# Optimization experiments

Measured on AMD Instinct MI355X. Metric: run time of the kernel, lower is better.

Reference implementation:

```python
import jax, jax.numpy as jnp
import numpy as np

N_NODES = 20000
N_EDGES = 240000
NUM_SPECIES = 4
NUM_BASIS = 16
MAX_RADIUS = 3.15
SQRT_NN = float(np.sqrt(12.0))  # num_neighbors normalization


def _cg121():
    # Clebsch-Gordan for 1e x 2e -> 1e in the real l=2 basis used below:
    # [xy, yz, (3z^2-1), zx, x^2-y^2] (component-normalized). Built from the
    # symmetric traceless matrix pairing M(a) @ v, normalized to unit Frobenius norm.
    s5, s15 = np.sqrt(5.0), np.sqrt(15.0)
    C = np.zeros((3, 5, 3))
    for A in range(5):
        a = np.zeros(5); a[A] = 1.0
        M = np.zeros((3, 3))
        M[0, 1] = M[1, 0] = a[0] * s15 / 2
        M[1, 2] = M[2, 1] = a[1] * s15 / 2
        M[0, 2] = M[2, 0] = a[3] * s15 / 2
        M[0, 0] = -a[2] * s5 / 2 + a[4] * s15 / 2
        M[1, 1] = -a[2] * s5 / 2 - a[4] * s15 / 2
        M[2, 2] = a[2] * s5
        C[:, A, :] = M
    C /= np.linalg.norm(C)
    return jnp.asarray(C, dtype=jnp.float32)

CG121 = _cg121()


def silu(v):
    return v * jax.nn.sigmoid(v)


def lin0(h, W):  # equivariant linear on scalars: [N,u] x [u,v]
    return h @ W / np.sqrt(W.shape[0])


def lin1(h, W):  # equivariant linear on vectors: [N,u,3] x [u,v]
    return jnp.einsum('nuk,uv->nvk', h, W) / np.sqrt(W.shape[0])


def radial_mlp(hb, W1, W2):  # FullyConnectedNet([16,64,nw], silu), normalized weights
    h = silu(hb @ W1 / np.sqrt(W1.shape[0]))
    return h @ W2 / np.sqrt(W2.shape[0])


def radial_basis(r):
    # soft_one_hot_linspace(..., basis='smooth_finite', cutoff=True) * sqrt(NUM_BASIS)
    values = np.linspace(0.0, MAX_RADIUS, NUM_BASIS + 2, dtype=np.float32)[1:-1]
    step = float(values[1] - values[0])
    d = (r[:, None] - values) / step
    def sus(t):
        safe = jnp.where(t > 0, t, 1.0)
        return jnp.where(t > 0, jnp.exp(-1.0 / safe), 0.0)
    y = 1.14136 * float(np.exp(2.0)) * sus(1.0 + d) * sus(1.0 - d)
    return y * np.sqrt(float(NUM_BASIS))


def sph_harm(edge_vec):
    # normalize=True, normalization='component' real spherical harmonics, l=0,1,2
    r = jnp.linalg.norm(edge_vec, axis=1)
    u = edge_vec / r[:, None]
    ux, uy, uz = u[:, 0], u[:, 1], u[:, 2]
    sh1 = np.sqrt(3.0) * u
    sh2 = jnp.stack([np.sqrt(15.0) * ux * uy,
                     np.sqrt(15.0) * uy * uz,
                     np.sqrt(5.0) / 2 * (3 * uz * uz - 1.0),
                     np.sqrt(15.0) * uz * ux,
                     np.sqrt(15.0) / 2 * (ux * ux - uy * uy)], axis=1)
    return r, sh1, sh2


def _forward(x, edge_index, edge_vec, emb,
             L1_lin1_0, L1_W1, L1_W2, L1_lin2_0, L1_lin2_1, L1_sc_0,
             L2_lin1_0, L2_lin1_1, L2_W1, L2_W2, L2_lin2_0, L2_lin2_1, L2_sc_0, L2_sc_1,
             LO_lin1_0, LO_lin1_1, LO_W1, LO_W2, LO_lin2_0, LO_sc_0):
    src, dst = edge_index[0], edge_index[1]
    N = x.shape[0]
    h0 = emb[x]                                   # [N,64] node embedding
    r, sh1, sh2 = sph_harm(edge_vec)
    hb = radial_basis(r)                          # [E,16]

    # ---- interaction 1: 64x0e -> (144x0e + 16x1e) -> gate -> 128x0e + 16x1e
    sc0 = lin0(h0, L1_sc_0)                       # self-connection [N,144]
    x0 = lin0(h0, L1_lin1_0)[src]                 # [E,64]
    w = radial_mlp(hb, L1_W1, L1_W2)              # [E,128] TP weights (uvu)
    m0 = x0 * w[:, :64]                           # 0e x 0e -> 0e
    m1 = (x0 * w[:, 64:128])[:, :, None] * sh1[:, None, :]  # 0e x 1e -> 1e
    a0 = jax.ops.segment_sum(m0, dst, num_segments=N) / SQRT_NN
    a1 = jax.ops.segment_sum(m1, dst, num_segments=N) / SQRT_NN
    g0 = lin0(a0, L1_lin2_0) + sc0                # [N,144]
    g1 = lin1(a1, L1_lin2_1)                      # [N,16,3]
    h0 = silu(g0[:, :128])                        # gated scalars
    h1 = jax.nn.sigmoid(g0[:, 128:])[:, :, None] * g1  # gate 16x1e

    # ---- interaction 2: 128x0e+16x1e -> (144x0e + 176x1e mid) -> gate
    sc0 = lin0(h0, L2_sc_0)                       # [N,144]
    sc1 = lin1(h1, L2_sc_1)                       # [N,16,3]
    x0 = lin0(h0, L2_lin1_0)[src]                 # [E,128]
    x1 = lin1(h1, L2_lin1_1)[src]                 # [E,16,3]
    w = radial_mlp(hb, L2_W1, L2_W2)              # [E,320]
    m0a = x0 * w[:, :128]                                            # 0x0->0
    m0b = jnp.einsum('euk,ek->eu', x1, sh1) / np.sqrt(3.0) * w[:, 272:288]  # 1x1->0
    m1a = (x0 * w[:, 128:256])[:, :, None] * sh1[:, None, :]         # 0x1->1
    m1b = x1 * w[:, 256:272][:, :, None]                             # 1x0->1
    m1c = jnp.cross(x1, sh1[:, None, :]) / np.sqrt(6.0) * w[:, 288:304][:, :, None]  # 1x1->1
    m1d = jnp.einsum('eui,eA,iAk->euk', x1, sh2, CG121) * w[:, 304:320][:, :, None]  # 1x2->1
    mid0 = jnp.concatenate([m0a, m0b], axis=1)    # [E,144]
    mid1 = jnp.concatenate([m1a, m1b, m1c, m1d], axis=1)  # [E,176,3]
    a0 = jax.ops.segment_sum(mid0, dst, num_segments=N) / SQRT_NN
    a1 = jax.ops.segment_sum(mid1, dst, num_segments=N) / SQRT_NN
    g0 = lin0(a0, L2_lin2_0) + sc0
    g1 = lin1(a1, L2_lin2_1) + sc1
    h0 = silu(g0[:, :128])
    h1 = jax.nn.sigmoid(g0[:, 128:])[:, :, None] * g1

    # ---- output interaction: -> 4x0e
    sc0 = lin0(h0, LO_sc_0)                       # [N,4]
    x0 = lin0(h0, LO_lin1_0)[src]
    x1 = lin1(h1, LO_lin1_1)[src]
    w = radial_mlp(hb, LO_W1, LO_W2)              # [E,144]
    m0a = x0 * w[:, :128]
    m0b = jnp.einsum('euk,ek->eu', x1, sh1) / np.sqrt(3.0) * w[:, 128:144]
    a0 = jax.ops.segment_sum(jnp.concatenate([m0a, m0b], axis=1), dst, num_segments=N) / SQRT_NN
    return lin0(a0, LO_lin2_0) + sc0              # [N,4]


def setup_inputs() -> dict:
    key = jax.random.key(0)
    ks = jax.random.split(key, 32)
    f = lambda i, shape: jax.random.normal(ks[i], shape, dtype=jnp.float32)
    return {
        'x': jax.random.randint(ks[0], (N_NODES,), 0, NUM_SPECIES),
        'edge_index': jax.random.randint(ks[1], (2, N_EDGES), 0, N_NODES),
        'edge_vec': jax.random.normal(ks[2], (N_EDGES, 3), dtype=jnp.float32),
        'emb': f(3, (NUM_SPECIES, 64)),
        'L1_lin1_0': f(4, (64, 64)),
        'L1_W1': f(5, (16, 64)), 'L1_W2': f(6, (64, 128)),
        'L1_lin2_0': f(7, (64, 144)), 'L1_lin2_1': f(8, (64, 16)),
        'L1_sc_0': f(9, (64, 144)),
        'L2_lin1_0': f(10, (128, 128)), 'L2_lin1_1': f(11, (16, 16)),
        'L2_W1': f(12, (16, 64)), 'L2_W2': f(13, (64, 320)),
        'L2_lin2_0': f(14, (144, 144)), 'L2_lin2_1': f(15, (176, 16)),
        'L2_sc_0': f(16, (128, 144)), 'L2_sc_1': f(17, (16, 16)),
        'LO_lin1_0': f(18, (128, 128)), 'LO_lin1_1': f(19, (16, 16)),
        'LO_W1': f(20, (16, 64)), 'LO_W2': f(21, (64, 144)),
        'LO_lin2_0': f(22, (144, 4)), 'LO_sc_0': f(23, (128, 4)),
    }


def reference(x, edge_index, edge_vec, emb,
              L1_lin1_0, L1_W1, L1_W2, L1_lin2_0, L1_lin2_1, L1_sc_0,
              L2_lin1_0, L2_lin1_1, L2_W1, L2_W2, L2_lin2_0, L2_lin2_1, L2_sc_0, L2_sc_1,
              LO_lin1_0, LO_lin1_1, LO_W1, LO_W2, LO_lin2_0, LO_sc_0):
    return _forward(x, edge_index, edge_vec, emb,
                    L1_lin1_0, L1_W1, L1_W2, L1_lin2_0, L1_lin2_1, L1_sc_0,
                    L2_lin1_0, L2_lin1_1, L2_W1, L2_W2, L2_lin2_0, L2_lin2_1, L2_sc_0, L2_sc_1,
                    LO_lin1_0, LO_lin1_1, LO_W1, LO_W2, LO_lin2_0, LO_sc_0)
```

## Files before the change

kernel.cpp:

```cpp
#include <hip/hip_runtime.h>
#include <math.h>

#define N_NODES 20000
#define N_EDGES 240000

typedef _Float16 half2_t __attribute__((ext_vector_type(2)));
typedef _Float16 f16x8   __attribute__((ext_vector_type(8)));
typedef float    f32x4v  __attribute__((ext_vector_type(4)));
typedef unsigned uint4v  __attribute__((ext_vector_type(4)));

__device__ __forceinline__ float siluf(float v){ return v * (1.0f/(1.0f+__expf(-v))); }
__device__ __forceinline__ float sigmf(float v){ return 1.0f/(1.0f+__expf(-v)); }

__device__ __forceinline__ unsigned pack_h2(float a, float b){
  half2_t h; h.x = (_Float16)a; h.y = (_Float16)b;
  return __builtin_bit_cast(unsigned, h);
}
__device__ __forceinline__ float dot2f(unsigned w, unsigned h, float acc){
#if __has_builtin(__builtin_amdgcn_fdot2)
  return __builtin_amdgcn_fdot2(__builtin_bit_cast(half2_t,w),
                                __builtin_bit_cast(half2_t,h), acc, false);
#else
  half2_t a = __builtin_bit_cast(half2_t,w), b = __builtin_bit_cast(half2_t,h);
  return acc + (float)a.x*(float)b.x + (float)a.y*(float)b.y;
#endif
}
__device__ __forceinline__ float dot8q(uint4v w, uint4v h, float acc){
  acc = dot2f(w.x, h.x, acc);
  acc = dot2f(w.y, h.y, acc);
  acc = dot2f(w.z, h.z, acc);
  return dot2f(w.w, h.w, acc);
}

__global__ void k_count(const int* __restrict__ ei, int* __restrict__ cnt){
  int e = blockIdx.x*blockDim.x + threadIdx.x;
  if (e < N_EDGES) atomicAdd(&cnt[ei[N_EDGES + e]], 1);
}

__global__ void k_scan(const int* __restrict__ cnt, int* __restrict__ off, int* __restrict__ pos){
  __shared__ int part[1024];
  int t = threadIdx.x;
  int c[20]; int s = 0;
  #pragma unroll
  for (int j=0;j<20;j++){
    int idx = t*20 + j;
    int v = (idx < N_NODES) ? cnt[idx] : 0;
    c[j] = s; s += v;
  }
  part[t] = s;
  __syncthreads();
  for (int d=1; d<1024; d<<=1){
    int add = (t>=d) ? part[t-d] : 0;
    __syncthreads();
    part[t] += add;
    __syncthreads();
  }
  int excl = part[t] - s;
  #pragma unroll
  for (int j=0;j<20;j++){
    int idx = t*20 + j;
    if (idx < N_NODES){ off[idx] = excl + c[j]; pos[idx] = excl + c[j]; }
  }
  if (t == 1023) off[N_NODES] = part[1023];
}

__global__ void k_scatter(const int* __restrict__ ei, int* __restrict__ pos,
                          int* __restrict__ perm, int* __restrict__ srcs){
  int e = blockIdx.x*blockDim.x + threadIdx.x;
  if (e >= N_EDGES) return;
  int d = ei[N_EDGES + e];
  int p = atomicAdd(&pos[d], 1);
  perm[e] = p;
  srcs[p] = ei[e];
}

__global__ void k_geom(const float* __restrict__ ev, const int* __restrict__ perm,
                       float* __restrict__ eg){
  int e = blockIdx.x*blockDim.x + threadIdx.x;
  if (e >= N_EDGES) return;
  float x = ev[3*e+0], y = ev[3*e+1], z = ev[3*e+2];
  float r = sqrtf(x*x + y*y + z*z);
  float inv = 1.0f / fmaxf(r, 1e-12f);
  float ux = x*inv, uy = y*inv, uz = z*inv;
  float* o = eg + (size_t)perm[e]*24;
  o[0] = 1.7320508f*ux; o[1] = 1.7320508f*uy; o[2] = 1.7320508f*uz;
  o[3] = 3.8729833f*ux*uy;
  o[4] = 3.8729833f*uy*uz;
  o[5] = 1.1180340f*(3.0f*uz*uz - 1.0f);
  o[6] = 3.8729833f*uz*ux;
  o[7] = 1.9364917f*(ux*ux - uy*uy);
  const float invstep = 17.0f/3.15f;
  float t = r*invstep;
  #pragma unroll
  for (int i=0;i<16;i++){
    float d = t - (float)(i+1);
    float a = 1.0f + d, b = 1.0f - d;
    float v = 0.0f;
    if (a > 0.0f && b > 0.0f) v = 33.734292f*__expf(-1.0f/a - 1.0f/b);
    o[8+i] = v;
  }
}

__global__ void k_packw(const float* __restrict__ Wu,
                        const float* __restrict__ Ws,  const float* __restrict__ Wl,
                        const float* __restrict__ Wlo, const float* __restrict__ Wso,
                        unsigned* __restrict__ WPu,
                        unsigned* __restrict__ WPs,  unsigned* __restrict__ WPl,
                        unsigned* __restrict__ WPlo, unsigned* __restrict__ WPso){
  int i = blockIdx.x*blockDim.x + threadIdx.x;
  const float f12 = 1.0f/12.0f;
  const float is128 = 0.08838835f;
  if (i < 144*72){
    int t = i/72, k2 = i%72;
    WPu[i] = pack_h2(Wu[(2*k2)*144+t]*f12, Wu[(2*k2+1)*144+t]*f12);
  } else if (i < 144*72 + 144*64){
    int ii = i - 144*72; int t = ii/64, k2 = ii%64;
    WPs[ii] = pack_h2(Ws[(2*k2)*144+t]*is128, Ws[(2*k2+1)*144+t]*is128);
  } else if (i < 144*72 + 144*64 + 128*64){
    int ii = i - 144*72 - 144*64; int t = ii/64, k2 = ii%64;
    WPl[ii] = pack_h2(Wl[(2*k2)*128+t]*is128, Wl[(2*k2+1)*128+t]*is128);
  } else if (i < 144*72 + 144*64 + 128*64 + 128*64){
    int ii = i - 144*72 - 144*64 - 128*64; int t = ii/64, k2 = ii%64;
    WPlo[ii] = pack_h2(Wlo[(2*k2)*128+t]*is128, Wlo[(2*k2+1)*128+t]*is128);
  } else if (i < 144*72 + 144*64 + 128*64 + 128*64 + 4*64){
    int ii = i - 144*72 - 144*64 - 128*64 - 128*64; int t = ii/64, k2 = ii%64;
    WPso[ii] = pack_h2(Wso[(2*k2)*4+t]*is128, Wso[(2*k2+1)*4+t]*is128);
  }
}

__global__ void k_node_l1(const int* __restrict__ xs, const float* __restrict__ emb,
                          const float* __restrict__ Wlin, const float* __restrict__ Wsc,
                          _Float16* __restrict__ X0, float* __restrict__ SC0){
  __shared__ float hs[4][64];
  int n0 = blockIdx.x*4;
  int t  = threadIdx.x;
  {
    int j = t>>6, k = t&63;
    hs[j][k] = emb[xs[n0+j]*64 + k];
  }
  __syncthreads();
  if (t < 64){
    float acc[4] = {};
    for (int k=0;k<64;k++){
      float wv = Wlin[k*64 + t];
      #pragma unroll
      for (int j=0;j<4;j++) acc[j] += hs[j][k]*wv;
    }
    #pragma unroll
    for (int j=0;j<4;j++) X0[(size_t)(n0+j)*64 + t] = (_Float16)(acc[j]*0.125f);
  } else if (t < 208){
    int o = t - 64;
    float acc[4] = {};
    for (int k=0;k<64;k++){
      float wv = Wsc[k*144 + o];
      #pragma unroll
      for (int j=0;j<4;j++) acc[j] += hs[j][k]*wv;
    }
    #pragma unroll
    for (int j=0;j<4;j++) SC0[(size_t)(n0+j)*144 + o] = acc[j]*0.125f;
  }
}

__global__ __launch_bounds__(256) void k_hidden(
    const float* __restrict__ EG, const float* __restrict__ W1,
    _Float16* __restrict__ H){
  __shared__ float w1s[16*64];
  int tid = threadIdx.x;
  for (int i=tid;i<16*64;i+=256) w1s[i] = W1[i]*0.25f;
  __syncthreads();
  int lane = tid & 63, wib = tid >> 6;
  int gw = blockIdx.x*4 + wib, nw = gridDim.x*4;
  for (int e = gw; e < N_EDGES; e += nw){
    const float* g8 = EG + (size_t)e*24 + 8;
    float a0 = 0.0f, a1 = 0.0f;
    #pragma unroll
    for (int b=0;b<8;b++){
      a0 = fmaf(g8[b],   w1s[b*64 + lane],     a0);
      a1 = fmaf(g8[8+b], w1s[(8+b)*64 + lane], a1);
    }
    H[(size_t)e*64 + lane] = (_Float16)siluf(a0 + a1);
  }
}

template<int MODE>
__device__ __forceinline__ float colscale(int c){
  if constexpr (MODE == 1){
    if (c >= 272 && c < 288) return 0.57735027f;
    if (c >= 288 && c < 304) return 0.40824829f;
    return 1.0f;
  } else if constexpr (MODE == 2){
    return (c >= 128) ? 0.57735027f : 1.0f;
  }
  return 1.0f;
}

template<int NT, int MODE>
__global__ __launch_bounds__(256) void k_ww_mfma(
    int e0c, int e1c, const _Float16* __restrict__ H,
    const float* __restrict__ W2, _Float16* __restrict__ WW){
  constexpr int NCOL = NT*16;
  constexpr int NTW  = (NT + 3) / 4;
  int tid = threadIdx.x;
  int lane = tid & 63, wib = tid >> 6;
  int row = lane & 15, quad = lane >> 4;
  const float fold = 0.125f*0.28867513f;
  f16x8 B0[NTW], B1[NTW];
  #pragma unroll
  for (int t2=0; t2<NTW; t2++){
    int ct = wib*NTW + t2;
    int c  = ct*16 + row;
    bool valid = (ct < NT);
    float fs = valid ? fold*colscale<MODE>(c) : 0.0f;
    int ci = valid ? c : 0;
    #pragma unroll
    for (int j=0;j<8;j++){
      B0[t2][j] = (_Float16)(W2[(quad*8+j)*NCOL + ci]*fs);
      B1[t2][j] = (_Float16)(W2[(32+quad*8+j)*NCOL + ci]*fs);
    }
  }
  int ntiles = (e1c - e0c) >> 4;
  for (int t = blockIdx.x; t < ntiles; t += gridDim.x){
    int eb = e0c + t*16;
    const _Float16* hp = H + (size_t)(eb + row)*64 + quad*8;
    f16x8 A0 = *(const f16x8*)hp;
    f16x8 A1 = *(const f16x8*)(hp + 32);
    #pragma unroll
    for (int t2=0; t2<NTW; t2++){
      int ct = wib*NTW + t2;
      f32x4v d = __builtin_amdgcn_mfma_f32_16x16x32_f16(A0, B0[t2], (f32x4v){0.f,0.f,0.f,0.f}, 0,0,0);
      d = __builtin_amdgcn_mfma_f32_16x16x32_f16(A1, B1[t2], d, 0,0,0);
      if (ct < NT){
        int c0 = ct*16;
        #pragma unroll
        for (int j=0;j<4;j++){
          WW[(size_t)(eb - e0c + quad*4 + j)*NCOL + c0 + row] = (_Float16)d[j];
        }
      }
    }
  }
}

__global__ __launch_bounds__(256) void k_gather_l1(
    const int* __restrict__ off, const int* __restrict__ srcs, const float* __restrict__ eg,
    const _Float16* __restrict__ WW, const _Float16* __restrict__ X0,
    float* __restrict__ A0, float* __restrict__ A1, int e0, int e1, int first){
  int tid = threadIdx.x, lane = tid & 63;
  int gw = (blockIdx.x*256 + tid) >> 6;
  int nw = (gridDim.x*256) >> 6;
  for (int n = gw; n < N_NODES; n += nw){
    int ib = off[n], ie = off[n+1];
    if (ib < e0) ib = e0;
    if (ie > e1) ie = e1;
    if (!first && ib >= ie) continue;
    float a0a = 0.0f, a1a[3] = {0,0,0};
    if (ib < ie){
      int src = srcs[ib];
      for (int i = ib; i < ie; i++){
        float x0 = (float)X0[(size_t)src*64 + lane];
        if (i+1 < ie) src = srcs[i+1];
        const float* g = eg + (size_t)i*24;
        const _Float16* w = WW + (size_t)(i - e0)*128;
        float w0  = (float)w[lane];
        float w1v = (float)w[64 + lane];
        float m0 = x0*w0, m1 = x0*w1v;
        a0a += m0;
        a1a[0] += m1*g[0]; a1a[1] += m1*g[1]; a1a[2] += m1*g[2];
      }
    }
    float* p = A1 + (size_t)n*192 + lane*3;
    if (first){
      A0[(size_t)n*64 + lane] = a0a;
      p[0] = a1a[0]; p[1] = a1a[1]; p[2] = a1a[2];
    } else {
      A0[(size_t)n*64 + lane] += a0a;
      p[0] += a1a[0]; p[1] += a1a[1]; p[2] += a1a[2];
    }
  }
}

__global__ __launch_bounds__(256) void k_gather_l2(
    const int* __restrict__ off, const int* __restrict__ srcs, const float* __restrict__ eg,
    const _Float16* __restrict__ WW, const _Float16* __restrict__ X0, const _Float16* __restrict__ X1,
    float* __restrict__ A0, float* __restrict__ A1, int e0, int e1, int first){
  int tid = threadIdx.x, lane = tid & 63;
  int grp = lane >> 4, v = lane & 15;
  int gw = (blockIdx.x*256 + tid) >> 6;
  int nw = (gridDim.x*256) >> 6;
  for (int n = gw; n < N_NODES; n += nw){
    int ib = off[n], ie = off[n+1];
    if (ib < e0) ib = e0;
    if (ie > e1) ie = e1;
    if (!first && ib >= ie) continue;
    float a0a=0.f, a0b=0.f, a0c=0.f;
    float a1a[3]={0,0,0}, a1b[3]={0,0,0}, a1g[3]={0,0,0};
    if (ib < ie){
      int src = srcs[ib];
      for (int i = ib; i < ie; i++){
        const _Float16* x0p = X0 + (size_t)src*128;
        float x0a = (float)x0p[lane], x0b = (float)x0p[64 + lane];
        const _Float16* x1p = X1 + (size_t)src*48 + v*3;
        float xx = (float)x1p[0], xy = (float)x1p[1], xz = (float)x1p[2];
        if (i+1 < ie) src = srcs[i+1];
        const float* g = eg + (size_t)i*24;
        const _Float16* w = WW + (size_t)(i - e0)*320;
        float w0  = (float)w[lane];
        float w1v = (float)w[ 64 + lane];
        float w2v = (float)w[128 + lane];
        float w3v = (float)w[192 + lane];
        float w4  = (float)w[256 + lane];
        float sx = g[0], sy = g[1], sz = g[2];
        a0a += x0a*w0;
        a0b += x0b*w1v;
        float ma = x0a*w2v, mb = x0b*w3v;
        a1a[0] += ma*sx; a1a[1] += ma*sy; a1a[2] += ma*sz;
        a1b[0] += mb*sx; a1b[1] += mb*sy; a1b[2] += mb*sz;
        if (grp == 0){
          a1g[0] += w4*xx; a1g[1] += w4*xy; a1g[2] += w4*xz;
        } else if (grp == 1){
          a0c += w4*(xx*sx + xy*sy + xz*sz);
        } else if (grp == 2){
          a1g[0] += w4*(xy*sz - xz*sy);
          a1g[1] += w4*(xz*sx - xx*sz);
          a1g[2] += w4*(xx*sy - xy*sx);
        } else {
          float s20=g[3], s21=g[4], s22=g[5], s23=g[6], s24=g[7];
          const float c1c = 0.31622777f, c2c = 0.18257419f;
          a1g[0] += w4*(xx*(c1c*s24 - c2c*s22) + xy*(c1c*s20)            + xz*(c1c*s23));
          a1g[1] += w4*(xx*(c1c*s20)           + xy*(-c2c*s22 - c1c*s24) + xz*(c1c*s21));
          a1g[2] += w4*(xx*(c1c*s23)           + xy*(c1c*s21)            + xz*(2.0f*c2c*s22));
        }
      }
    }
    float* a0 = A0 + (size_t)n*144;
    float* a1 = A1 + (size_t)n*528;
    int gbase = (grp == 0) ? 128 : (grp == 2) ? 144 : (grp == 3) ? 160 : -1;
    if (first){
      a0[lane] = a0a;
      a0[64 + lane] = a0b;
      if (grp == 1) a0[128 + v] = a0c;
      float* p = a1 + lane*3;
      p[0] = a1a[0]; p[1] = a1a[1]; p[2] = a1a[2];
      p = a1 + (64 + lane)*3;
      p[0] = a1b[0]; p[1] = a1b[1]; p[2] = a1b[2];
      if (gbase >= 0){
        p = a1 + (gbase + v)*3;
        p[0] = a1g[0]; p[1] = a1g[1]; p[2] = a1g[2];
      }
    } else {
      a0[lane] += a0a;
      a0[64 + lane] += a0b;
      if (grp == 1) a0[128 + v] += a0c;
      float* p = a1 + lane*3;
      p[0] += a1a[0]; p[1] += a1a[1]; p[2] += a1a[2];
      p = a1 + (64 + lane)*3;
      p[0] += a1b[0]; p[1] += a1b[1]; p[2] += a1b[2];
      if (gbase >= 0){
        p = a1 + (gbase + v)*3;
        p[0] += a1g[0]; p[1] += a1g[1]; p[2] += a1g[2];
      }
    }
  }
}

__global__ __launch_bounds__(256) void k_gather_lo(
    const int* __restrict__ off, const int* __restrict__ srcs, const float* __restrict__ eg,
    const _Float16* __restrict__ WW, const _Float16* __restrict__ X0, const _Float16* __restrict__ X1,
    float* __restrict__ A0, int e0, int e1, int first){
  int tid = threadIdx.x, lane = tid & 63, v = lane & 15;
  int gw = (blockIdx.x*256 + tid) >> 6;
  int nw = (gridDim.x*256) >> 6;
  for (int n = gw; n < N_NODES; n += nw){
    int ib = off[n], ie = off[n+1];
    if (ib < e0) ib = e0;
    if (ie > e1) ie = e1;
    if (!first && ib >= ie) continue;
    float a0a = 0.f, a0b = 0.f, a0c = 0.f;
    if (ib < ie){
      int src = srcs[ib];
      for (int i = ib; i < ie; i++){
        const _Float16* x0p = X0 + (size_t)src*128;
        float x0a = (float)x0p[lane], x0b = (float)x0p[64 + lane];
        const _Float16* x1p = X1 + (size_t)src*48 + v*3;
        float xx = (float)x1p[0], xy = (float)x1p[1], xz = (float)x1p[2];
        if (i+1 < ie) src = srcs[i+1];
        const float* g = eg + (size_t)i*24;
        const _Float16* w = WW + (size_t)(i - e0)*144;
        float w0  = (float)w[lane];
        float w1v = (float)w[64 + lane];
        float w2v = (float)w[128 + v];
        a0a += x0a*w0;
        a0b += x0b*w1v;
        float dot = xx*g[0] + xy*g[1] + xz*g[2];
        a0c += w2v*dot;
      }
    }
    float* a0 = A0 + (size_t)n*144;
    if (first){
      a0[lane] = a0a;
      a0[64 + lane] = a0b;
      if (lane < 16) a0[128 + lane] = a0c;
    } else {
      a0[lane] += a0a;
      a0[64 + lane] += a0b;
      if (lane < 16) a0[128 + lane] += a0c;
    }
  }
}

__global__ __launch_bounds__(256) void k_upd_l1(
    const float* __restrict__ A0, const float* __restrict__ A1,
    const float* __restrict__ SC0,
    const float* __restrict__ W20, const float* __restrict__ W21,
    float* __restrict__ H0, float* __restrict__ H1){
  __shared__ float a0s[8*64];
  __shared__ float a1s[8*192];
  __shared__ float w21s[64*16];
  __shared__ float sig[8][16];
  __shared__ float g1s[8][48];
  int n0 = blockIdx.x*8, t = threadIdx.x;
  {
    const float4* s0 = (const float4*)(A0 + (size_t)n0*64);
    float4* d0 = (float4*)a0s;
    for (int i=t;i<8*64/4;i+=256) d0[i] = s0[i];
    const float4* s1 = (const float4*)(A1 + (size_t)n0*192);
    float4* d1 = (float4*)a1s;
    for (int i=t;i<8*192/4;i+=256) d1[i] = s1[i];
    const float4* sw = (const float4*)W21;
    float4* dw = (float4*)w21s;
    for (int i=t;i<64*16/4;i+=256) dw[i] = sw[i];
  }
  __syncthreads();
  if (t < 144){
    float acc[8] = {};
    for (int k=0;k<64;k++){
      float wv = W20[k*144 + t];
      #pragma unroll
      for (int j=0;j<8;j++) acc[j] += a0s[j*64 + k]*wv;
    }
    #pragma unroll
    for (int j=0;j<8;j++){
      float gg = acc[j]*0.125f + SC0[(size_t)(n0+j)*144 + t];
      if (t < 128) H0[(size_t)(n0+j)*128 + t] = siluf(gg);
      else         sig[j][t-128] = sigmf(gg);
    }
  } else if (t < 192){
    int idx = t-144, v = idx/3, k = idx%3;
    float acc[8] = {};
    for (int u=0;u<64;u++){
      float wv = w21s[u*16 + v];
      #pragma unroll
      for (int j=0;j<8;j++) acc[j] += a1s[j*192 + u*3 + k]*wv;
    }
    #pragma unroll
    for (int j=0;j<8;j++) g1s[j][idx] = acc[j]*0.125f;
  }
  __syncthreads();
  if (t >= 144 && t < 192){
    int idx = t-144, v = idx/3;
    #pragma unroll
    for (int j=0;j<8;j++) H1[(size_t)(n0+j)*48 + idx] = sig[j][v]*g1s[j][idx];
  }
}

__global__ __launch_bounds__(384) void k_lin_l2(
    const float* __restrict__ H0, const float* __restrict__ H1,
    const unsigned* __restrict__ WPs, const float* __restrict__ Wsc1,
    const unsigned* __restrict__ WPl, const float* __restrict__ Wl1,
    float* __restrict__ SC0, float* __restrict__ SC1,
    _Float16* __restrict__ X0,  _Float16* __restrict__ X1){
  __shared__ uint4v h0h8[128];
  __shared__ float h1s[8*48];
  int n0 = blockIdx.x*8, t = threadIdx.x;
  if (t < 128){
    const float4* s0 = (const float4*)(H0 + (size_t)n0*128);
    float4 f0 = s0[t*2], f1 = s0[t*2+1];
    uint4v u;
    u.x = pack_h2(f0.x, f0.y); u.y = pack_h2(f0.z, f0.w);
    u.z = pack_h2(f1.x, f1.y); u.w = pack_h2(f1.z, f1.w);
    h0h8[t] = u;
  } else if (t < 224){
    int i = t - 128;
    const float4* s1 = (const float4*)(H1 + (size_t)n0*48);
    if (i < 96) ((float4*)h1s)[i] = s1[i];
  }
  __syncthreads();
  const uint4v* wps4 = (const uint4v*)WPs;
  const uint4v* wpl4 = (const uint4v*)WPl;
  if (t < 144){
    float acc[8] = {};
    for (int kq=0;kq<16;kq++){
      uint4v wq = wps4[t*16 + kq];
      #pragma unroll
      for (int j=0;j<8;j++){
        uint4v av = h0h8[j*16 + kq];
        acc[j] = dot8q(wq, av, acc[j]);
      }
    }
    #pragma unroll
    for (int j=0;j<8;j++) SC0[(size_t)(n0+j)*144 + t] = acc[j];
  } else if (t < 192){
    int idx = t-144, v = idx/3, k = idx%3;
    float acc[8] = {};
    for (int u=0;u<16;u++){
      float wv = Wsc1[u*16 + v];
      #pragma unroll
      for (int j=0;j<8;j++) acc[j] += h1s[j*48 + u*3 + k]*wv;
    }
    #pragma unroll
    for (int j=0;j<8;j++) SC1[(size_t)(n0+j)*48 + idx] = acc[j]*0.25f;
  } else if (t < 320){
    int o = t-192;
    float acc[8] = {};
    for (int kq=0;kq<16;kq++){
      uint4v wq = wpl4[o*16 + kq];
      #pragma unroll
      for (int j=0;j<8;j++){
        uint4v av = h0h8[j*16 + kq];
        acc[j] = dot8q(wq, av, acc[j]);
      }
    }
    #pragma unroll
    for (int j=0;j<8;j++) X0[(size_t)(n0+j)*128 + o] = (_Float16)acc[j];
  } else if (t < 368){
    int idx = t-320, v = idx/3, k = idx%3;
    float acc[8] = {};
    for (int u=0;u<16;u++){
      float wv = Wl1[u*16 + v];
      #pragma unroll
      for (int j=0;j<8;j++) acc[j] += h1s[j*48 + u*3 + k]*wv;
    }
    #pragma unroll
    for (int j=0;j<8;j++) X1[(size_t)(n0+j)*48 + idx] = (_Float16)(acc[j]*0.25f);
  }
}

__global__ __launch_bounds__(256) void k_upd_l2(
    const float* __restrict__ A0, const float* __restrict__ A1,
    const float* __restrict__ SC0, const float* __restrict__ SC1,
    const unsigned* __restrict__ WPu, const float* __restrict__ W21,
    float* __restrict__ H0, float* __restrict__ H1){
  __shared__ uint4v a0h8[144];
  __shared__ float a1s[8*528];
  __shared__ float sig[8][16];
  __shared__ float g1s[8][48];
  int n0 = blockIdx.x*8, t = threadIdx.x;
  if (t < 144){
    const float4* s0 = (const float4*)(A0 + (size_t)n0*144);
    float4 f0 = s0[t*2], f1 = s0[t*2+1];
    uint4v u;
    u.x = pack_h2(f0.x, f0.y); u.y = pack_h2(f0.z, f0.w);
    u.z = pack_h2(f1.x, f1.y); u.w = pack_h2(f1.z, f1.w);
    a0h8[t] = u;
  }
  {
    const float4* s1 = (const float4*)(A1 + (size_t)n0*528);
    float4* d1 = (float4*)a1s;
    for (int i=t;i<8*528/4;i+=256) d1[i] = s1[i];
  }
  __syncthreads();
  const uint4v* wpu4 = (const uint4v*)WPu;
  if (t < 144){
    float acc[8] = {};
    for (int kq=0;kq<18;kq++){
      uint4v wq = wpu4[t*18 + kq];
      #pragma unroll
      for (int j=0;j<8;j++){
        uint4v av = a0h8[j*18 + kq];
        acc[j] = dot8q(wq, av, acc[j]);
      }
    }
    #pragma unroll
    for (int j=0;j<8;j++){
      float gg = acc[j] + SC0[(size_t)(n0+j)*144 + t];
      if (t < 128) H0[(size_t)(n0+j)*128 + t] = siluf(gg);
      else         sig[j][t-128] = sigmf(gg);
    }
  } else if (t < 192){
    int idx = t-144, v = idx/3, k = idx%3;
    float acc[8] = {};
    for (int u=0;u<176;u++){
      float wv = W21[u*16 + v];
      #pragma unroll
      for (int j=0;j<8;j++) acc[j] += a1s[j*528 + u*3 + k]*wv;
    }
    #pragma unroll
    for (int j=0;j<8;j++) g1s[j][idx] = acc[j]*0.075377836f + SC1[(size_t)(n0+j)*48 + idx];
  }
  __syncthreads();
  if (t >= 144 && t < 192){
    int idx = t-144, v = idx/3;
    #pragma unroll
    for (int j=0;j<8;j++) H1[(size_t)(n0+j)*48 + idx] = sig[j][v]*g1s[j][idx];
  }
}

__global__ __launch_bounds__(256) void k_lin_lo(
    const float* __restrict__ H0, const float* __restrict__ H1,
    const unsigned* __restrict__ WPso,
    const unsigned* __restrict__ WPlo, const float* __restrict__ Wl1,
    float* __restrict__ SCO, _Float16* __restrict__ X0, _Float16* __restrict__ X1){
  __shared__ uint4v h0h8[128];
  __shared__ float h1s[8*48];
  int n0 = blockIdx.x*8, t = threadIdx.x;
  if (t < 128){
    const float4* s0 = (const float4*)(H0 + (size_t)n0*128);
    float4 f0 = s0[t*2], f1 = s0[t*2+1];
    uint4v u;
    u.x = pack_h2(f0.x, f0.y); u.y = pack_h2(f0.z, f0.w);
    u.z = pack_h2(f1.x, f1.y); u.w = pack_h2(f1.z, f1.w);
    h0h8[t] = u;
  } else if (t < 224){
    int i = t - 128;
    const float4* s1 = (const float4*)(H1 + (size_t)n0*48);
    if (i < 96) ((float4*)h1s)[i] = s1[i];
  }
  __syncthreads();
  const uint4v* wso4 = (const uint4v*)WPso;
  const uint4v* wlo4 = (const uint4v*)WPlo;
  if (t < 4){
    float acc[8] = {};
    for (int kq=0;kq<16;kq++){
      uint4v wq = wso4[t*16 + kq];
      #pragma unroll
      for (int j=0;j<8;j++){
        uint4v av = h0h8[j*16 + kq];
        acc[j] = dot8q(wq, av, acc[j]);
      }
    }
    #pragma unroll
    for (int j=0;j<8;j++) SCO[(size_t)(n0+j)*4 + t] = acc[j];
  } else if (t < 132){
    int o = t-4;
    float acc[8] = {};
    for (int kq=0;kq<16;kq++){
      uint4v wq = wlo4[o*16 + kq];
      #pragma unroll
      for (int j=0;j<8;j++){
        uint4v av = h0h8[j*16 + kq];
        acc[j] = dot8q(wq, av, acc[j]);
      }
    }
    #pragma unroll
    for (int j=0;j<8;j++) X0[(size_t)(n0+j)*128 + o] = (_Float16)acc[j];
  } else if (t < 180){
    int idx = t-132, v = idx/3, k = idx%3;
    float acc[8] = {};
    for (int u=0;u<16;u++){
      float wv = Wl1[u*16 + v];
      #pragma unroll
      for (int j=0;j<8;j++) acc[j] += h1s[j*48 + u*3 + k]*wv;
    }
    #pragma unroll
    for (int j=0;j<8;j++) X1[(size_t)(n0+j)*48 + idx] = (_Float16)(acc[j]*0.25f);
  }
}

__global__ __launch_bounds__(256) void k_final(
    const float* __restrict__ A0, const float* __restrict__ SCO,
    const float* __restrict__ W, float* __restrict__ out){
  __shared__ float a0s[32*144];
  int n0 = blockIdx.x*32, t = threadIdx.x;
  {
    const float4* s0 = (const float4*)(A0 + (size_t)n0*144);
    float4* d0 = (float4*)a0s;
    for (int i=t;i<32*144/4;i+=256) d0[i] = s0[i];
  }
  __syncthreads();
  if (t < 128){
    int j = t >> 2, c = t & 3;
    float acc = 0.0f;
    for (int k=0;k<144;k++) acc += a0s[j*144 + k]*W[k*4 + c];
    int i = (n0 + j)*4 + c;
    out[i] = acc*(1.0f/12.0f) + SCO[i];
  }
}

extern "C" void kernel_launch(void* const* d_in, const int* in_sizes, int n_in,
                              void* d_out, int out_size, void* d_ws, size_t ws_size,
                              hipStream_t stream) {
  const int*   x   = (const int*)  d_in[0];
  const int*   ei  = (const int*)  d_in[1];
  const float* ev  = (const float*)d_in[2];
  const float* emb = (const float*)d_in[3];
  const float* L1_lin1_0 = (const float*)d_in[4];
  const float* L1_W1     = (const float*)d_in[5];
  const float* L1_W2     = (const float*)d_in[6];
  const float* L1_lin2_0 = (const float*)d_in[7];
  const float* L1_lin2_1 = (const float*)d_in[8];
  const float* L1_sc_0   = (const float*)d_in[9];
  const float* L2_lin1_0 = (const float*)d_in[10];
  const float* L2_lin1_1 = (const float*)d_in[11];
  const float* L2_W1     = (const float*)d_in[12];
  const float* L2_W2     = (const float*)d_in[13];
  const float* L2_lin2_0 = (const float*)d_in[14];
  const float* L2_lin2_1 = (const float*)d_in[15];
  const float* L2_sc_0   = (const float*)d_in[16];
  const float* L2_sc_1   = (const float*)d_in[17];
  const float* LO_lin1_0 = (const float*)d_in[18];
  const float* LO_lin1_1 = (const float*)d_in[19];
  const float* LO_W1     = (const float*)d_in[20];
  const float* LO_W2     = (const float*)d_in[21];
  const float* LO_lin2_0 = (const float*)d_in[22];
  const float* LO_sc_0   = (const float*)d_in[23];
  float* out = (float*)d_out;

  int* cnt  = (int*)d_ws;
  int* off  = cnt  + N_NODES;
  int* pos  = off  + N_NODES + 1;
  int* perm = pos  + N_NODES;
  int* srcs = perm + N_EDGES;
  float* EG  = (float*)(((char*)d_ws) + ((size_t)540004 * 4));
  _Float16* X0 = (_Float16*)(EG + (size_t)N_EDGES*24);
  _Float16* X1 = (_Float16*)(X0 + (size_t)N_NODES*128);
  float* SC0 = (float*)(((char*)(X1 + (size_t)N_NODES*48)) + 0);
  float* SC1 = SC0 + (size_t)N_NODES*144;
  float* A0  = SC1 + (size_t)N_NODES*48;
  float* A1  = A0  + (size_t)N_NODES*144;
  float* H0  = A1  + (size_t)N_NODES*528;
  float* H1  = H0  + (size_t)N_NODES*128;
  _Float16* HH = (_Float16*)(H1 + (size_t)N_NODES*48);
  unsigned* WPu  = (unsigned*)(HH + (size_t)N_EDGES*64);
  unsigned* WPs  = WPu  + 144*72;
  unsigned* WPl  = WPs  + 144*64;
  unsigned* WPlo = WPl  + 128*64;
  unsigned* WPso = WPlo + 128*64;
  _Float16* WW = (_Float16*)(WPso + 4*64);

  size_t used = (size_t)((char*)WW - (char*)d_ws);
  size_t avail = (ws_size > used) ? (ws_size - used) : 0;
  auto chunk_for = [&](int ncol)->int{
    size_t ce = avail / ((size_t)ncol * sizeof(_Float16));
    if (ce >= (size_t)N_EDGES) return N_EDGES;
    int c = (int)ce & ~15;
    return c < 4096 ? 4096 : c;
  };

  hipMemsetAsync(cnt, 0, N_NODES*sizeof(int), stream);
  k_count  <<<(N_EDGES+255)/256, 256, 0, stream>>>(ei, cnt);
  k_scan   <<<1, 1024, 0, stream>>>(cnt, off, pos);
  k_scatter<<<(N_EDGES+255)/256, 256, 0, stream>>>(ei, pos, perm, srcs);
  k_geom   <<<(N_EDGES+255)/256, 256, 0, stream>>>(ev, perm, EG);
  k_packw  <<<142, 256, 0, stream>>>(L2_lin2_0, L2_sc_0, L2_lin1_0,
                                     LO_lin1_0, LO_sc_0,
                                     WPu, WPs, WPl, WPlo, WPso);

  k_node_l1<<<N_NODES/4, 256, 0, stream>>>(x, emb, L1_lin1_0, L1_sc_0, X0, SC0);
  k_hidden<<<2048, 256, 0, stream>>>(EG, L1_W1, HH);
  {
    int chunk = chunk_for(128);
    for (int e0 = 0; e0 < N_EDGES; e0 += chunk){
      int e1 = (e0 + chunk < N_EDGES) ? e0 + chunk : N_EDGES;
      k_ww_mfma<8,0><<<2048, 256, 0, stream>>>(e0, e1, HH, L1_W2, WW);
      k_gather_l1<<<5000, 256, 0, stream>>>(off, srcs, EG, WW, X0, A0, A1, e0, e1, e0==0);
    }
  }
  k_upd_l1<<<N_NODES/8, 256, 0, stream>>>(A0, A1, SC0, L1_lin2_0, L1_lin2_1, H0, H1);

  k_lin_l2<<<N_NODES/8, 384, 0, stream>>>(H0, H1, WPs, L2_sc_1, WPl, L2_lin1_1,
                                          SC0, SC1, X0, X1);
  k_hidden<<<2048, 256, 0, stream>>>(EG, L2_W1, HH);
  {
    int chunk = chunk_for(320);
    for (int e0 = 0; e0 < N_EDGES; e0 += chunk){
      int e1 = (e0 + chunk < N_EDGES) ? e0 + chunk : N_EDGES;
      k_ww_mfma<20,1><<<2048, 256, 0, stream>>>(e0, e1, HH, L2_W2, WW);
      k_gather_l2<<<5000, 256, 0, stream>>>(off, srcs, EG, WW, X0, X1, A0, A1, e0, e1, e0==0);
    }
  }
  k_upd_l2<<<N_NODES/8, 256, 0, stream>>>(A0, A1, SC0, SC1, WPu, L2_lin2_1, H0, H1);

  k_lin_lo<<<N_NODES/8, 256, 0, stream>>>(H0, H1, WPso, WPlo, LO_lin1_1, SC1, X0, X1);
  k_hidden<<<2048, 256, 0, stream>>>(EG, LO_W1, HH);
  {
    int chunk = chunk_for(144);
    for (int e0 = 0; e0 < N_EDGES; e0 += chunk){
      int e1 = (e0 + chunk < N_EDGES) ? e0 + chunk : N_EDGES;
      k_ww_mfma<9,2><<<2048, 256, 0, stream>>>(e0, e1, HH, LO_W2, WW);
      k_gather_lo<<<5000, 256, 0, stream>>>(off, srcs, EG, WW, X0, X1, A0, e0, e1, e0==0);
    }
  }
  k_final<<<N_NODES/32, 256, 0, stream>>>(A0, SC1, LO_lin2_0, out);
}
```

Baseline: 623.6 us.

## Interleave fp16 node and edge-weight layouts for paired loads in gathers

Node features X0 are stored with the two 64-channel halves interleaved, X1 vectors are padded to 4 halves, and the MFMA edge-weight writer interleaves column blocks in pairs. This lets the gather kernels fetch two fp16 values with one 32-bit load (or 64-bit for X1) instead of separate scalar half loads. The l=2 spherical harmonics are also precomputed in k_geom as the symmetric CG matrix entries, which removes per-lane arithmetic in the gather. The cost is a larger X1 buffer and scattered 16-bit stores in the MFMA and node kernels.

```diff
diff --git a/kernel.cpp b/kernel.cpp
--- a/kernel.cpp
+++ b/kernel.cpp
@@ -15,6 +15,10 @@
 __device__ __forceinline__ unsigned pack_h2(float a, float b){
   half2_t h; h.x = (_Float16)a; h.y = (_Float16)b;
   return __builtin_bit_cast(unsigned, h);
+}
+__device__ __forceinline__ float2 unpack_h2(unsigned u){
+  half2_t h = __builtin_bit_cast(half2_t, u);
+  return make_float2((float)h.x, (float)h.y);
 }
 __device__ __forceinline__ float dot2f(unsigned w, unsigned h, float acc){
 #if __has_builtin(__builtin_amdgcn_fdot2)
@@ -84,11 +88,17 @@
   float ux = x*inv, uy = y*inv, uz = z*inv;
   float* o = eg + (size_t)perm[e]*24;
   o[0] = 1.7320508f*ux; o[1] = 1.7320508f*uy; o[2] = 1.7320508f*uz;
-  o[3] = 3.8729833f*ux*uy;
-  o[4] = 3.8729833f*uy*uz;
-  o[5] = 1.1180340f*(3.0f*uz*uz - 1.0f);
-  o[6] = 3.8729833f*uz*ux;
-  o[7] = 1.9364917f*(ux*ux - uy*uy);
+  float s20 = 3.8729833f*ux*uy;
+  float s21 = 3.8729833f*uy*uz;
+  float s22 = 1.1180340f*(3.0f*uz*uz - 1.0f);
+  float s23 = 3.8729833f*uz*ux;
+  float s24 = 1.9364917f*(ux*ux - uy*uy);
+  const float c1 = 0.31622777f, c2 = 0.18257419f;
+  o[3] = c1*s24 - c2*s22;
+  o[4] = c1*s20;
+  o[5] = c1*s23;
+  o[6] = c1*s21;
+  o[7] = 2.0f*c2*s22;
   const float invstep = 17.0f/3.15f;
   float t = r*invstep;
   #pragma unroll
@@ -199,6 +209,7 @@
     int e0c, int e1c, const _Float16* __restrict__ H,
     const float* __restrict__ W2, _Float16* __restrict__ WW){
   constexpr int NCOL = NT*16;
+  constexpr int NPAIR = (NCOL/64)/2;
   constexpr int NTW  = (NT + 3) / 4;
   int tid = threadIdx.x;
   int lane = tid & 63, wib = tid >> 6;
@@ -230,10 +241,14 @@
       f32x4v d = __builtin_amdgcn_mfma_f32_16x16x32_f16(A0, B0[t2], (f32x4v){0.f,0.f,0.f,0.f}, 0,0,0);
       d = __builtin_amdgcn_mfma_f32_16x16x32_f16(A1, B1[t2], d, 0,0,0);
       if (ct < NT){
-        int c0 = ct*16;
+        int b = ct >> 2;
+        int within = (ct & 3)*16 + row;
+        int woff;
+        if (b < 2*NPAIR) woff = (b>>1)*128 + within*2 + (b&1);
+        else             woff = NPAIR*128 + (b - 2*NPAIR)*64 + within;
         #pragma unroll
         for (int j=0;j<4;j++){
-          WW[(size_t)(eb - e0c + quad*4 + j)*NCOL + c0 + row] = (_Float16)d[j];
+          WW[(size_t)(eb - e0c + quad*4 + j)*NCOL + woff] = (_Float16)d[j];
         }
       }
     }
@@ -259,10 +274,9 @@
         float x0 = (float)X0[(size_t)src*64 + lane];
         if (i+1 < ie) src = srcs[i+1];
         const float* g = eg + (size_t)i*24;
-        const _Float16* w = WW + (size_t)(i - e0)*128;
-        float w0  = (float)w[lane];
-        float w1v = (float)w[64 + lane];
-        float m0 = x0*w0, m1 = x0*w1v;
+        const unsigned* wr = (const unsigned*)(WW + (size_t)(i - e0)*128);
+        float2 w01 = unpack_h2(wr[lane]);
+        float m0 = x0*w01.x, m1 = x0*w01.y;
         a0a += m0;
         a1a[0] += m1*g[0]; a1a[1] += m1*g[1]; a1a[2] += m1*g[2];
       }
@@ -296,22 +310,21 @@
     if (ib < ie){
       int src = srcs[ib];
       for (int i = ib; i < ie; i++){
-        const _Float16* x0p = X0 + (size_t)src*128;
-        float x0a = (float)x0p[lane], x0b = (float)x0p[64 + lane];
-        const _Float16* x1p = X1 + (size_t)src*48 + v*3;
-        float xx = (float)x1p[0], xy = (float)x1p[1], xz = (float)x1p[2];
+        float2 x0p = unpack_h2(((const unsigned*)(X0 + (size_t)src*128))[lane]);
+        uint2 x1u = ((const uint2*)(X1 + (size_t)src*64))[v];
+        float2 xab = unpack_h2(x1u.x);
+        float2 xcp = unpack_h2(x1u.y);
+        float xx = xab.x, xy = xab.y, xz = xcp.x;
         if (i+1 < ie) src = srcs[i+1];
         const float* g = eg + (size_t)i*24;
-        const _Float16* w = WW + (size_t)(i - e0)*320;
-        float w0  = (float)w[lane];
-        float w1v = (float)w[ 64 + lane];
-        float w2v = (float)w[128 + lane];
-        float w3v = (float)w[192 + lane];
-        float w4  = (float)w[256 + lane];
+        const unsigned* wr = (const unsigned*)(WW + (size_t)(i - e0)*320);
+        float2 w01 = unpack_h2(wr[lane]);
+        float2 w23 = unpack_h2(wr[64 + lane]);
+        float w4 = (float)((const _Float16*)wr)[256 + lane];
         float sx = g[0], sy = g[1], sz = g[2];
-        a0a += x0a*w0;
-        a0b += x0b*w1v;
-        float ma = x0a*w2v, mb = x0b*w3v;
+        a0a += x0p.x*w01.x;
+        a0b += x0p.y*w01.y;
+        float ma = x0p.x*w23.x, mb = x0p.y*w23.y;
         a1a[0] += ma*sx; a1a[1] += ma*sy; a1a[2] += ma*sz;
         a1b[0] += mb*sx; a1b[1] += mb*sy; a1b[2] += mb*sz;
         if (grp == 0){
@@ -323,11 +336,11 @@
           a1g[1] += w4*(xz*sx - xx*sz);
           a1g[2] += w4*(xx*sy - xy*sx);
         } else {
-          float s20=g[3], s21=g[4], s22=g[5], s23=g[6], s24=g[7];
-          const float c1c = 0.31622777f, c2c = 0.18257419f;
-          a1g[0] += w4*(xx*(c1c*s24 - c2c*s22) + xy*(c1c*s20)            + xz*(c1c*s23));
-          a1g[1] += w4*(xx*(c1c*s20)           + xy*(-c2c*s22 - c1c*s24) + xz*(c1c*s21));
-          a1g[2] += w4*(xx*(c1c*s23)           + xy*(c1c*s21)            + xz*(2.0f*c2c*s22));
+          float M00=g[3], M01=g[4], M02=g[5], M12=g[6], M22=g[7];
+          float M11 = -(M00 + M22);
+          a1g[0] += w4*(xx*M00 + xy*M01 + xz*M02);
+          a1g[1] += w4*(xx*M01 + xy*M11 + xz*M12);
+          a1g[2] += w4*(xx*M02 + xy*M12 + xz*M22);
         }
       }
     }
@@ -378,19 +391,18 @@
     if (ib < ie){
       int src = srcs[ib];
       for (int i = ib; i < ie; i++){
-        const _Float16* x0p = X0 + (size_t)src*128;
-        float x0a = (float)x0p[lane], x0b = (float)x0p[64 + lane];
-        const _Float16* x1p = X1 + (size_t)src*48 + v*3;
-        float xx = (float)x1p[0], xy = (float)x1p[1], xz = (float)x1p[2];
+        float2 x0p = unpack_h2(((const unsigned*)(X0 + (size_t)src*128))[lane]);
+        uint2 x1u = ((const uint2*)(X1 + (size_t)src*64))[v];
+        float2 xab = unpack_h2(x1u.x);
+        float2 xcp = unpack_h2(x1u.y);
         if (i+1 < ie) src = srcs[i+1];
         const float* g = eg + (size_t)i*24;
-        const _Float16* w = WW + (size_t)(i - e0)*144;
-        float w0  = (float)w[lane];
-        float w1v = (float)w[64 + lane];
-        float w2v = (float)w[128 + v];
-        a0a += x0a*w0;
-        a0b += x0b*w1v;
-        float dot = xx*g[0] + xy*g[1] + xz*g[2];
+        const unsigned* wr = (const unsigned*)(WW + (size_t)(i - e0)*144);
+        float2 w01 = unpack_h2(wr[lane]);
+        float w2v = (float)((const _Float16*)wr)[128 + v];
+        a0a += x0p.x*w01.x;
+        a0b += x0p.y*w01.y;
+        float dot = xab.x*g[0] + xab.y*g[1] + xcp.x*g[2];
         a0c += w2v*dot;
       }
     }
@@ -520,7 +532,7 @@
       }
     }
     #pragma unroll
-    for (int j=0;j<8;j++) X0[(size_t)(n0+j)*128 + o] = (_Float16)acc[j];
+    for (int j=0;j<8;j++) X0[(size_t)(n0+j)*128 + (o&63)*2 + (o>>6)] = (_Float16)acc[j];
   } else if (t < 368){
     int idx = t-320, v = idx/3, k = idx%3;
     float acc[8] = {};
@@ -530,7 +542,7 @@
       for (int j=0;j<8;j++) acc[j] += h1s[j*48 + u*3 + k]*wv;
     }
     #pragma unroll
-    for (int j=0;j<8;j++) X1[(size_t)(n0+j)*48 + idx] = (_Float16)(acc[j]*0.25f);
+    for (int j=0;j<8;j++) X1[(size_t)(n0+j)*64 + v*4 + k] = (_Float16)(acc[j]*0.25f);
   }
 }
 
@@ -641,7 +653,7 @@
       }
     }
     #pragma unroll
-    for (int j=0;j<8;j++) X0[(size_t)(n0+j)*128 + o] = (_Float16)acc[j];
+    for (int j=0;j<8;j++) X0[(size_t)(n0+j)*128 + (o&63)*2 + (o>>6)] = (_Float16)acc[j];
   } else if (t < 180){
     int idx = t-132, v = idx/3, k = idx%3;
     float acc[8] = {};
@@ -651,7 +663,7 @@
       for (int j=0;j<8;j++) acc[j] += h1s[j*48 + u*3 + k]*wv;
     }
     #pragma unroll
-    for (int j=0;j<8;j++) X1[(size_t)(n0+j)*48 + idx] = (_Float16)(acc[j]*0.25f);
+    for (int j=0;j<8;j++) X1[(size_t)(n0+j)*64 + v*4 + k] = (_Float16)(acc[j]*0.25f);
   }
 }
 
@@ -712,7 +724,7 @@
   float* EG  = (float*)(((char*)d_ws) + ((size_t)540004 * 4));
   _Float16* X0 = (_Float16*)(EG + (size_t)N_EDGES*24);
   _Float16* X1 = (_Float16*)(X0 + (size_t)N_NODES*128);
-  float* SC0 = (float*)(((char*)(X1 + (size_t)N_NODES*48)) + 0);
+  float* SC0 = (float*)(X1 + (size_t)N_NODES*64);
   float* SC1 = SC0 + (size_t)N_NODES*144;
   float* A0  = SC1 + (size_t)N_NODES*48;
   float* A1  = A0  + (size_t)N_NODES*144;
```

New measurement: 632.2 us. About the same (+1.4%).
